# Performance work log

Measured on AMD Instinct MI355X. Metric: run time of the kernel, lower is better.

The kernel has to match this reference:

```python
import jax, jax.numpy as jnp
import numpy as np
from math import sqrt

B, P, D = 4, 2048, 1024
H, DK = 16, 64  # n_heads, d_keys


def setup_inputs() -> dict:
    key = jax.random.key(0)
    ks = jax.random.split(key, 6)
    s = 1.0 / sqrt(D)
    return {
        "target_embedding": jax.random.normal(ks[0], (B, P, D), dtype=jnp.float32),
        "Wq": jax.random.normal(ks[1], (D, H * DK), dtype=jnp.float32) * s,
        "bq": jnp.zeros((H * DK,), dtype=jnp.float32),
        "Wk": jax.random.normal(ks[2], (D, H * DK), dtype=jnp.float32) * s,
        "bk": jnp.zeros((H * DK,), dtype=jnp.float32),
        "Wv": jax.random.normal(ks[3], (D, H * DK), dtype=jnp.float32) * s,
        "bv": jnp.zeros((H * DK,), dtype=jnp.float32),
        "Wo": jax.random.normal(ks[4], (H * DK, D), dtype=jnp.float32) * s,
        "bo": jnp.zeros((D,), dtype=jnp.float32),
    }


def reference(target_embedding, Wq, bq, Wk, bk, Wv, bv, Wo, bo):
    x = target_embedding
    b, p, _ = x.shape
    # QKV projections -> [B, P, H, DK]
    q = (x @ Wq + bq).reshape(b, p, H, DK)
    k = (x @ Wk + bk).reshape(b, p, H, DK)
    v = (x @ Wv + bv).reshape(b, p, H, DK)
    scale = 1.0 / sqrt(DK)
    scores = jnp.einsum("bphd,bqhd->bhpq", q, k)  # [B, H, P, P]
    A = jax.nn.softmax(scale * scores, axis=-1)  # dropout is identity in eval
    rep = jnp.einsum("bhpq,bqhd->bphd", A, v).reshape(b, p, H * DK)
    return rep @ Wo + bo
```

## Files before the change

### kernel.cpp

```cpp
#include <hip/hip_runtime.h>

typedef __attribute__((ext_vector_type(8))) short short8;
typedef __attribute__((ext_vector_type(4))) short short4v;
typedef __attribute__((ext_vector_type(4))) float f32x4;
typedef __attribute__((ext_vector_type(4))) unsigned short ushort4v;
typedef __attribute__((ext_vector_type(2))) unsigned int uint2v;

#define GLOBAL_AS __attribute__((address_space(1)))
#define LDS_AS    __attribute__((address_space(3)))

__device__ __forceinline__ unsigned short f2bf(float f) {
    unsigned int u = __float_as_uint(f);
    u += 0x7fffu + ((u >> 16) & 1u);
    return (unsigned short)(u >> 16);
}

__device__ __forceinline__ unsigned int pack_rhu(float a, float b) {
    unsigned int ua = __float_as_uint(a) + 0x8000u;
    unsigned int ub = __float_as_uint(b) + 0x8000u;
    return __builtin_amdgcn_perm(ub, ua, 0x07060302u);
}

__device__ __forceinline__ short4v pack4_rhu(float p0, float p1, float p2, float p3) {
    uint2v uu;
    uu[0] = pack_rhu(p0, p1);
    uu[1] = pack_rhu(p2, p3);
    return __builtin_bit_cast(short4v, uu);
}

__device__ __forceinline__ float fexp2(float x) {
    return __builtin_amdgcn_exp2f(x);
}

__device__ __forceinline__ void async_cp16(void* lds, const void* g) {
    __builtin_amdgcn_global_load_lds((GLOBAL_AS unsigned int*)g,
                                     (LDS_AS unsigned int*)lds, 16, 0, 0);
}

#define SCL2E 0.18033688011112042591999058512524f

__global__ void prep_kernel(const float* __restrict__ X,
                            const float* __restrict__ Wq,
                            const float* __restrict__ Wk,
                            const float* __restrict__ Wv,
                            const float* __restrict__ Wo,
                            unsigned short* __restrict__ Xb,
                            unsigned short* __restrict__ Wts) {
    const int z = blockIdx.z;
    if (z < 4) {
        __shared__ float tile[32][33];
        const float* src = (z == 0) ? Wq : (z == 1) ? Wk : (z == 2) ? Wv : Wo;
        unsigned short* dst = Wts + z * 1048576;
        const int tx = threadIdx.x, ty = threadIdx.y;
        const int x0 = blockIdx.x * 32, y0 = blockIdx.y * 32;
#pragma unroll
        for (int i = 0; i < 32; i += 8)
            tile[ty + i][tx] = src[(y0 + ty + i) * 1024 + x0 + tx];
        __syncthreads();
#pragma unroll
        for (int i = 0; i < 32; i += 8)
            dst[(x0 + ty + i) * 1024 + y0 + tx] = f2bf(tile[tx][ty + i]);
    } else {
        const int tid = threadIdx.y * 32 + threadIdx.x;
        const int chunk = blockIdx.y * 32 + blockIdx.x;
        const int base = chunk * 8192;
#pragma unroll
        for (int pass = 0; pass < 8; ++pass) {
            int i = base + pass * 1024 + tid * 4;
            float4 v = *(const float4*)&X[i];
            ushort4v o;
            o.x = f2bf(v.x); o.y = f2bf(v.y); o.z = f2bf(v.z); o.w = f2bf(v.w);
            *(ushort4v*)&Xb[i] = o;
        }
    }
}

__global__ void transpose_v_kernel(const unsigned short* __restrict__ V,
                                   unsigned short* __restrict__ Vt) {
    __shared__ unsigned short tile[32][33];
    const int bh = blockIdx.z;
    const int p0 = blockIdx.x * 32, d0 = blockIdx.y * 32;
    const unsigned short* src = V + bh * (2048 * 64);
    unsigned short* dst = Vt + bh * (2048 * 64);
    const int tx = threadIdx.x, ty = threadIdx.y;
#pragma unroll
    for (int i = 0; i < 32; i += 8)
        tile[ty + i][tx] = src[(p0 + ty + i) * 64 + d0 + tx];
    __syncthreads();
#pragma unroll
    for (int i = 0; i < 32; i += 8)
        dst[(d0 + ty + i) * 2048 + p0 + tx] = tile[tx][ty + i];
}

__device__ __forceinline__ void gemm_mainloop_128(
    const unsigned short* __restrict__ A, const unsigned short* __restrict__ Bt,
    int m0, int n0, unsigned short* As, unsigned short* Bs, f32x4 acc[4][4]) {
    const int tid = threadIdx.x;
    const int lane = tid & 63;
    const int wave = tid >> 6;
    const int wr = wave >> 1, wc = wave & 1;
    const int c = lane & 15, quad = lane >> 4;

#pragma unroll
    for (int mt = 0; mt < 4; ++mt)
#pragma unroll
        for (int nt = 0; nt < 4; ++nt)
            acc[mt][nt] = (f32x4)0.0f;

    for (int k0 = 0; k0 < 1024; k0 += 32) {
#pragma unroll
        for (int i = 0; i < 2; ++i) {
            int s = tid + 256 * i;
            int r = s >> 2, gp = s & 3;
            int g = gp ^ ((r >> 1) & 3);
            async_cp16(&As[s * 8], &A[(m0 + r) * 1024 + k0 + g * 8]);
        }
#pragma unroll
        for (int i = 0; i < 2; ++i) {
            int s = tid + 256 * i;
            int r = s >> 2, gp = s & 3;
            int g = gp ^ ((r >> 1) & 3);
            async_cp16(&Bs[s * 8], &Bt[(n0 + r) * 1024 + k0 + g * 8]);
        }
        asm volatile("s_waitcnt vmcnt(0)" ::: "memory");
        __syncthreads();

        short8 af[4], bf[4];
#pragma unroll
        for (int mt = 0; mt < 4; ++mt) {
            int r = wr * 64 + mt * 16 + c;
            int gp = quad ^ ((r >> 1) & 3);
            af[mt] = *(const short8*)&As[r * 32 + gp * 8];
        }
#pragma unroll
        for (int nt = 0; nt < 4; ++nt) {
            int r = wc * 64 + nt * 16 + c;
            int gp = quad ^ ((r >> 1) & 3);
            bf[nt] = *(const short8*)&Bs[r * 32 + gp * 8];
        }
#pragma unroll
        for (int mt = 0; mt < 4; ++mt)
#pragma unroll
            for (int nt = 0; nt < 4; ++nt)
                acc[mt][nt] = __builtin_amdgcn_mfma_f32_16x16x32_bf16(
                    af[mt], bf[nt], acc[mt][nt], 0, 0, 0);
        __syncthreads();
    }
}

__global__ __launch_bounds__(256, 3) void gemm_qkv_kernel(
    const unsigned short* __restrict__ Xb, const unsigned short* __restrict__ Wts,
    const float* __restrict__ bq, const float* __restrict__ bk,
    const float* __restrict__ bv, unsigned short* __restrict__ Qb,
    unsigned short* __restrict__ Kb, unsigned short* __restrict__ Vb) {
    __shared__ __align__(16) unsigned short As[128 * 32];
    __shared__ __align__(16) unsigned short Bs[128 * 32];
    const int z = blockIdx.z;
    const unsigned short* Bt = Wts + z * 1048576;
    const float* bias = (z == 0) ? bq : (z == 1) ? bk : bv;
    const int m0 = blockIdx.y * 128, n0 = blockIdx.x * 128;
    f32x4 acc[4][4];
    gemm_mainloop_128(Xb, Bt, m0, n0, As, Bs, acc);

    const int lane = threadIdx.x & 63, wave = threadIdx.x >> 6;
    const int wr = wave >> 1, wc = wave & 1;
    const int c = lane & 15, quad = lane >> 4;
    unsigned short* dst = (z == 0) ? Qb : (z == 1) ? Kb : Vb;
    const float qscale = (z == 0) ? SCL2E : 1.0f;
#pragma unroll
    for (int nt = 0; nt < 4; ++nt) {
        int col = n0 + wc * 64 + nt * 16 + c;
        float bb = bias[col];
        int h = col >> 6, dk = col & 63;
#pragma unroll
        for (int mt = 0; mt < 4; ++mt) {
#pragma unroll
            for (int r = 0; r < 4; ++r) {
                int row = m0 + wr * 64 + mt * 16 + quad * 4 + r;
                int b = row >> 11, p = row & 2047;
                float v = (acc[mt][nt][r] + bb) * qscale;
                dst[((b * 16 + h) * 2048 + p) * 64 + dk] = f2bf(v);
            }
        }
    }
}

__device__ __forceinline__ void load_kv_regs(
    const unsigned short* __restrict__ Kbh, const unsigned short* __restrict__ Vbh,
    int k0, int tid, short8 kr[2], short8 vr[2]) {
#pragma unroll
    for (int i = 0; i < 2; ++i) {
        int s = tid + 256 * i;
        int r = s >> 3, gp = s & 7;
        int g = gp ^ (r & 7);
        kr[i] = *(const short8*)&Kbh[(k0 + r) * 64 + g * 8];
        vr[i] = *(const short8*)&Vbh[r * 2048 + k0 + g * 8];
    }
}

__global__ __launch_bounds__(256, 2) void attn_kernel(
    const unsigned short* __restrict__ Q, const unsigned short* __restrict__ K,
    const unsigned short* __restrict__ Vt, unsigned short* __restrict__ rep) {
    __shared__ __align__(16) unsigned short SMEM[16384];
    const int tid = threadIdx.x, lane = tid & 63, wave = tid >> 6;
    const int c = lane & 15, quad = lane >> 4;
    const int bh = blockIdx.y;
    const int q0 = blockIdx.x * 256 + wave * 64;
    const unsigned short* Qbh = Q + bh * (2048 * 64);
    const unsigned short* Kbh = K + bh * (2048 * 64);
    const unsigned short* Vbh = Vt + bh * (64 * 2048);

    short8 qf[4][2];
#pragma unroll
    for (int t = 0; t < 4; ++t)
#pragma unroll
        for (int ks = 0; ks < 2; ++ks)
            qf[t][ks] = *(const short8*)&Qbh[(q0 + t * 16 + c) * 64 + ks * 32 + quad * 8];

    short8 kr[2], vr[2];
    load_kv_regs(Kbh, Vbh, 0, tid, kr, vr);

    f32x4 o[4][4];
    float lpart[4] = {0.0f, 0.0f, 0.0f, 0.0f};
#pragma unroll
    for (int t = 0; t < 4; ++t)
#pragma unroll
        for (int d = 0; d < 4; ++d) o[t][d] = (f32x4)0.0f;

    for (int it = 0; it < 32; ++it) {
        const int buf = it & 1;
        unsigned short* Ksb = &SMEM[buf * 4096];
        unsigned short* Vsb = &SMEM[8192 + buf * 4096];
#pragma unroll
        for (int i = 0; i < 2; ++i) {
            int s = tid + 256 * i;
            *(short8*)&Ksb[s * 8] = kr[i];
            *(short8*)&Vsb[s * 8] = vr[i];
        }
        __syncthreads();
        if (it < 31)
            load_kv_regs(Kbh, Vbh, (it + 1) * 64, tid, kr, vr);

        short8 kf[4][2];
#pragma unroll
        for (int nt = 0; nt < 4; ++nt)
#pragma unroll
            for (int ks = 0; ks < 2; ++ks) {
                int r = nt * 16 + c;
                int gp2 = (quad + 4 * ks) ^ (r & 7);
                kf[nt][ks] = *(const short8*)&Ksb[r * 64 + gp2 * 8];
            }

        short4v vf[4][4];
#pragma unroll
        for (int dkt = 0; dkt < 4; ++dkt) {
            int r = dkt * 16 + c;
#pragma unroll
            for (int kt = 0; kt < 4; ++kt) {
                int gbase = 2 * kt + (quad >> 1);
                int g = gbase ^ (r & 7);
                int eloff = g * 8 + (quad & 1) * 4;
                vf[dkt][kt] = *(const short4v*)&Vsb[r * 64 + eloff];
            }
        }

        f32x4 zc = (f32x4)0.0f;
        zc = __builtin_amdgcn_mfma_f32_16x16x32_bf16(kf[0][0], qf[0][0], zc, 0, 0, 0);
        zc = __builtin_amdgcn_mfma_f32_16x16x32_bf16(kf[0][1], qf[0][1], zc, 0, 0, 0);
#pragma unroll
        for (int u = 0; u < 16; ++u) {
            const int t = u >> 2, nt = u & 3;
            f32x4 zn = (f32x4)0.0f;
            if (u < 15) {
                const int t2 = (u + 1) >> 2, nt2 = (u + 1) & 3;
                zn = __builtin_amdgcn_mfma_f32_16x16x32_bf16(kf[nt2][0], qf[t2][0], zn, 0, 0, 0);
                zn = __builtin_amdgcn_mfma_f32_16x16x32_bf16(kf[nt2][1], qf[t2][1], zn, 0, 0, 0);
            }
            float p0 = fexp2(zc[0]), p1 = fexp2(zc[1]);
            float p2 = fexp2(zc[2]), p3 = fexp2(zc[3]);
            lpart[t] += (p0 + p1) + (p2 + p3);
            short4v pf = pack4_rhu(p0, p1, p2, p3);
#pragma unroll
            for (int dkt = 0; dkt < 4; ++dkt)
                o[t][dkt] = __builtin_amdgcn_mfma_f32_16x16x16bf16_1k(
                    vf[dkt][nt], pf, o[t][dkt], 0, 0, 0);
            zc = zn;
        }
    }

    float inv[4];
#pragma unroll
    for (int t = 0; t < 4; ++t) {
        float l = lpart[t];
        l += __shfl_xor(l, 16);
        l += __shfl_xor(l, 32);
        inv[t] = 1.0f / l;
    }

    __syncthreads();
    const int b = bh >> 4, h = bh & 15;
    unsigned short* ob = &SMEM[wave * 2304];
#pragma unroll
    for (int pass = 0; pass < 2; ++pass) {
#pragma unroll
        for (int th = 0; th < 2; ++th) {
            int t = pass * 2 + th;
#pragma unroll
            for (int dkt = 0; dkt < 4; ++dkt) {
                short4v frag = pack4_rhu(o[t][dkt][0] * inv[t], o[t][dkt][1] * inv[t],
                                         o[t][dkt][2] * inv[t], o[t][dkt][3] * inv[t]);
                *(short4v*)&ob[(th * 16 + c) * 72 + dkt * 16 + quad * 4] = frag;
            }
        }
        asm volatile("s_waitcnt lgkmcnt(0)" ::: "memory");
#pragma unroll
        for (int sp = 0; sp < 4; ++sp) {
            int qr = sp * 8 + (lane >> 3);
            int d8 = (lane & 7) * 8;
            short8 row = *(const short8*)&ob[qr * 72 + d8];
            *(short8*)&rep[(b * 2048 + q0 + pass * 32 + qr) * 1024 + h * 64 + d8] = row;
        }
    }
}

__global__ __launch_bounds__(256, 3) void gemm_out_kernel(
    const unsigned short* __restrict__ rep, const unsigned short* __restrict__ Wot,
    const float* __restrict__ bo, float* __restrict__ out) {
    __shared__ __align__(16) unsigned short As[128 * 32];
    __shared__ __align__(16) unsigned short Bs[128 * 32];
    const int m0 = blockIdx.y * 128, n0 = blockIdx.x * 128;
    f32x4 acc[4][4];
    gemm_mainloop_128(rep, Wot, m0, n0, As, Bs, acc);
    const int lane = threadIdx.x & 63, wave = threadIdx.x >> 6;
    const int wr = wave >> 1, wc = wave & 1;
    const int c = lane & 15, quad = lane >> 4;
#pragma unroll
    for (int nt = 0; nt < 4; ++nt) {
        int col = n0 + wc * 64 + nt * 16 + c;
        float bb = bo[col];
#pragma unroll
        for (int mt = 0; mt < 4; ++mt) {
            int row = m0 + wr * 64 + mt * 16 + quad * 4;
#pragma unroll
            for (int r = 0; r < 4; ++r)
                out[(row + r) * 1024 + col] = acc[mt][nt][r] + bb;
        }
    }
}

extern "C" void kernel_launch(void* const* d_in, const int* in_sizes, int n_in,
                              void* d_out, int out_size, void* d_ws, size_t ws_size,
                              hipStream_t stream) {
    (void)in_sizes; (void)n_in; (void)out_size; (void)ws_size;
    const float* X  = (const float*)d_in[0];
    const float* Wq = (const float*)d_in[1];
    const float* bq = (const float*)d_in[2];
    const float* Wk = (const float*)d_in[3];
    const float* bk = (const float*)d_in[4];
    const float* Wv = (const float*)d_in[5];
    const float* bv = (const float*)d_in[6];
    const float* Wo = (const float*)d_in[7];
    const float* bo = (const float*)d_in[8];
    float* out = (float*)d_out;

    char* ws = (char*)d_ws;
    unsigned short* Xb   = (unsigned short*)(ws);
    unsigned short* Wts  = (unsigned short*)(ws + (16u << 20));
    unsigned short* Qb   = (unsigned short*)(ws + (24u << 20));
    unsigned short* Kb   = (unsigned short*)(ws + (40u << 20));
    unsigned short* Vb   = (unsigned short*)(ws + (56u << 20));
    unsigned short* Vtb  = (unsigned short*)(ws);
    unsigned short* repb = (unsigned short*)(ws + (56u << 20));

    prep_kernel<<<dim3(32, 32, 5), dim3(32, 8), 0, stream>>>(X, Wq, Wk, Wv, Wo, Xb, Wts);
    gemm_qkv_kernel<<<dim3(8, 64, 3), 256, 0, stream>>>(Xb, Wts, bq, bk, bv, Qb, Kb, Vb);
    transpose_v_kernel<<<dim3(64, 2, 64), dim3(32, 8), 0, stream>>>(Vb, Vtb);
    attn_kernel<<<dim3(8, 64), 256, 0, stream>>>(Qb, Kb, Vtb, repb);
    gemm_out_kernel<<<dim3(8, 64), 256, 0, stream>>>(repb, Wts + 3 * 1048576, bo, out);
}
```

Baseline: 298.0 us.

## Fuse V transpose into QKV GEMM by computing V^T and padding V LDS tile

The V projection block now computes W^T·X^T by swapping operands, so it writes V already transposed and the separate transpose kernel launch goes away. The attention kernel loads V^T without the XOR swizzle and stores it in LDS with a 72-element padded row stride, which simplifies fragment addressing. The workspace buffers are reassigned so rep reuses the Xb region. The risk is that the transposed epilogue writes along p with a 2-byte scatter per lane, and the padding raises LDS use per block.

```diff
diff --git a/kernel.cpp b/kernel.cpp
--- a/kernel.cpp
+++ b/kernel.cpp
@@ -75,23 +75,6 @@
     }
 }
 
-__global__ void transpose_v_kernel(const unsigned short* __restrict__ V,
-                                   unsigned short* __restrict__ Vt) {
-    __shared__ unsigned short tile[32][33];
-    const int bh = blockIdx.z;
-    const int p0 = blockIdx.x * 32, d0 = blockIdx.y * 32;
-    const unsigned short* src = V + bh * (2048 * 64);
-    unsigned short* dst = Vt + bh * (2048 * 64);
-    const int tx = threadIdx.x, ty = threadIdx.y;
-#pragma unroll
-    for (int i = 0; i < 32; i += 8)
-        tile[ty + i][tx] = src[(p0 + ty + i) * 64 + d0 + tx];
-    __syncthreads();
-#pragma unroll
-    for (int i = 0; i < 32; i += 8)
-        dst[(d0 + ty + i) * 2048 + p0 + tx] = tile[tx][ty + i];
-}
-
 __device__ __forceinline__ void gemm_mainloop_128(
     const unsigned short* __restrict__ A, const unsigned short* __restrict__ Bt,
     int m0, int n0, unsigned short* As, unsigned short* Bs, f32x4 acc[4][4]) {
@@ -152,34 +135,63 @@
     const unsigned short* __restrict__ Xb, const unsigned short* __restrict__ Wts,
     const float* __restrict__ bq, const float* __restrict__ bk,
     const float* __restrict__ bv, unsigned short* __restrict__ Qb,
-    unsigned short* __restrict__ Kb, unsigned short* __restrict__ Vb) {
+    unsigned short* __restrict__ Kb, unsigned short* __restrict__ Vtb) {
     __shared__ __align__(16) unsigned short As[128 * 32];
     __shared__ __align__(16) unsigned short Bs[128 * 32];
     const int z = blockIdx.z;
-    const unsigned short* Bt = Wts + z * 1048576;
-    const float* bias = (z == 0) ? bq : (z == 1) ? bk : bv;
-    const int m0 = blockIdx.y * 128, n0 = blockIdx.x * 128;
+    const unsigned short* Wz = Wts + z * 1048576;
+    const bool swapped = (z == 2);
+    const int m0 = (swapped ? blockIdx.x : blockIdx.y) * 128;
+    const int n0 = (swapped ? blockIdx.y : blockIdx.x) * 128;
+    const unsigned short* Amat = swapped ? Wz : Xb;
+    const unsigned short* Bmat = swapped ? Xb : Wz;
     f32x4 acc[4][4];
-    gemm_mainloop_128(Xb, Bt, m0, n0, As, Bs, acc);
+    gemm_mainloop_128(Amat, Bmat, m0, n0, As, Bs, acc);
 
     const int lane = threadIdx.x & 63, wave = threadIdx.x >> 6;
     const int wr = wave >> 1, wc = wave & 1;
     const int c = lane & 15, quad = lane >> 4;
-    unsigned short* dst = (z == 0) ? Qb : (z == 1) ? Kb : Vb;
-    const float qscale = (z == 0) ? SCL2E : 1.0f;
-#pragma unroll
-    for (int nt = 0; nt < 4; ++nt) {
-        int col = n0 + wc * 64 + nt * 16 + c;
-        float bb = bias[col];
-        int h = col >> 6, dk = col & 63;
-#pragma unroll
-        for (int mt = 0; mt < 4; ++mt) {
-#pragma unroll
-            for (int r = 0; r < 4; ++r) {
-                int row = m0 + wr * 64 + mt * 16 + quad * 4 + r;
-                int b = row >> 11, p = row & 2047;
-                float v = (acc[mt][nt][r] + bb) * qscale;
-                dst[((b * 16 + h) * 2048 + p) * 64 + dk] = f2bf(v);
+
+    if (!swapped) {
+        const float* bias = (z == 0) ? bq : bk;
+        unsigned short* dst = (z == 0) ? Qb : Kb;
+        const float qscale = (z == 0) ? SCL2E : 1.0f;
+#pragma unroll
+        for (int nt = 0; nt < 4; ++nt) {
+            int col = n0 + wc * 64 + nt * 16 + c;
+            float bb = bias[col];
+            int h = col >> 6, dk = col & 63;
+#pragma unroll
+            for (int mt = 0; mt < 4; ++mt) {
+#pragma unroll
+                for (int r = 0; r < 4; ++r) {
+                    int row = m0 + wr * 64 + mt * 16 + quad * 4 + r;
+                    int b = row >> 11, p = row & 2047;
+                    float v = (acc[mt][nt][r] + bb) * qscale;
+                    dst[((b * 16 + h) * 2048 + p) * 64 + dk] = f2bf(v);
+                }
+            }
+        }
+    } else {
+        float bb2[4][4];
+#pragma unroll
+        for (int mt = 0; mt < 4; ++mt)
+#pragma unroll
+            for (int r = 0; r < 4; ++r)
+                bb2[mt][r] = bv[m0 + wr * 64 + mt * 16 + quad * 4 + r];
+#pragma unroll
+        for (int nt = 0; nt < 4; ++nt) {
+            int colp = n0 + wc * 64 + nt * 16 + c;
+            int b = colp >> 11, p = colp & 2047;
+#pragma unroll
+            for (int mt = 0; mt < 4; ++mt) {
+#pragma unroll
+                for (int r = 0; r < 4; ++r) {
+                    int rowv = m0 + wr * 64 + mt * 16 + quad * 4 + r;
+                    int h = rowv >> 6, dk = rowv & 63;
+                    float v = acc[mt][nt][r] + bb2[mt][r];
+                    Vtb[(b * 16 + h) * 131072 + dk * 2048 + p] = f2bf(v);
+                }
             }
         }
     }
@@ -194,14 +206,14 @@
         int r = s >> 3, gp = s & 7;
         int g = gp ^ (r & 7);
         kr[i] = *(const short8*)&Kbh[(k0 + r) * 64 + g * 8];
-        vr[i] = *(const short8*)&Vbh[r * 2048 + k0 + g * 8];
+        vr[i] = *(const short8*)&Vbh[r * 2048 + k0 + gp * 8];
     }
 }
 
 __global__ __launch_bounds__(256, 2) void attn_kernel(
     const unsigned short* __restrict__ Q, const unsigned short* __restrict__ K,
     const unsigned short* __restrict__ Vt, unsigned short* __restrict__ rep) {
-    __shared__ __align__(16) unsigned short SMEM[16384];
+    __shared__ __align__(16) unsigned short SMEM[17408];
     const int tid = threadIdx.x, lane = tid & 63, wave = tid >> 6;
     const int c = lane & 15, quad = lane >> 4;
     const int bh = blockIdx.y;
@@ -230,12 +242,13 @@
     for (int it = 0; it < 32; ++it) {
         const int buf = it & 1;
         unsigned short* Ksb = &SMEM[buf * 4096];
-        unsigned short* Vsb = &SMEM[8192 + buf * 4096];
+        unsigned short* Vsb = &SMEM[8192 + buf * 4608];
 #pragma unroll
         for (int i = 0; i < 2; ++i) {
             int s = tid + 256 * i;
+            int r = s >> 3, gp = s & 7;
             *(short8*)&Ksb[s * 8] = kr[i];
-            *(short8*)&Vsb[s * 8] = vr[i];
+            *(short8*)&Vsb[r * 72 + gp * 8] = vr[i];
         }
         __syncthreads();
         if (it < 31)
@@ -256,12 +269,8 @@
         for (int dkt = 0; dkt < 4; ++dkt) {
             int r = dkt * 16 + c;
 #pragma unroll
-            for (int kt = 0; kt < 4; ++kt) {
-                int gbase = 2 * kt + (quad >> 1);
-                int g = gbase ^ (r & 7);
-                int eloff = g * 8 + (quad & 1) * 4;
-                vf[dkt][kt] = *(const short4v*)&Vsb[r * 64 + eloff];
-            }
+            for (int kt = 0; kt < 4; ++kt)
+                vf[dkt][kt] = *(const short4v*)&Vsb[r * 72 + kt * 16 + quad * 4];
         }
 
         f32x4 zc = (f32x4)0.0f;
@@ -368,13 +377,11 @@
     unsigned short* Wts  = (unsigned short*)(ws + (16u << 20));
     unsigned short* Qb   = (unsigned short*)(ws + (24u << 20));
     unsigned short* Kb   = (unsigned short*)(ws + (40u << 20));
-    unsigned short* Vb   = (unsigned short*)(ws + (56u << 20));
-    unsigned short* Vtb  = (unsigned short*)(ws);
-    unsigned short* repb = (unsigned short*)(ws + (56u << 20));
+    unsigned short* Vtb  = (unsigned short*)(ws + (56u << 20));
+    unsigned short* repb = (unsigned short*)(ws);
 
     prep_kernel<<<dim3(32, 32, 5), dim3(32, 8), 0, stream>>>(X, Wq, Wk, Wv, Wo, Xb, Wts);
-    gemm_qkv_kernel<<<dim3(8, 64, 3), 256, 0, stream>>>(Xb, Wts, bq, bk, bv, Qb, Kb, Vb);
-    transpose_v_kernel<<<dim3(64, 2, 64), dim3(32, 8), 0, stream>>>(Vb, Vtb);
+    gemm_qkv_kernel<<<dim3(8, 64, 3), 256, 0, stream>>>(Xb, Wts, bq, bk, bv, Qb, Kb, Vtb);
     attn_kernel<<<dim3(8, 64), 256, 0, stream>>>(Qb, Kb, Vtb, repb);
     gemm_out_kernel<<<dim3(8, 64), 256, 0, stream>>>(repb, Wts + 3 * 1048576, bo, out);
 }
```

Measured after the change: 292.3 us. No clear change (-1.9%).
